# Kernel tuning notes

Hardware: AMD Instinct MI355X
Metric: run time of the kernel (lower is better)

The kernel has to match this reference:

```python
import jax, jax.numpy as jnp
import numpy as np

NUM_EMB = 100000
EMB = 64
NUM_CTNS = 10
HEADS = 4
ATT = 32
HD = HEADS * ATT  # 128
FIELDS = 32       # 20 onehot + 2 multihot + 10 ctns
B = 8192


def _linear_params(key, out_f, in_f):
    kw, kb = jax.random.split(key)
    W = jax.random.normal(kw, (out_f, in_f), jnp.float32) * 0.05
    b = jax.random.normal(kb, (out_f,), jnp.float32) * 0.05
    return W, b


def setup_inputs() -> dict:
    key = jax.random.key(0)
    ks = jax.random.split(key, 16)
    inp = {
        'onehot_i': jax.random.randint(ks[0], (B, 20), 0, NUM_EMB),
        'onehot_x': jax.random.uniform(ks[1], (B, 20), jnp.float32),
        'mh_i': jax.random.randint(ks[2], (2, B, 50), 0, NUM_EMB),
        'mh_x': jax.random.uniform(ks[3], (2, B, 50), jnp.float32),
        'ctns': jax.random.normal(ks[4], (B, NUM_CTNS), jnp.float32),
        'xx': jax.random.normal(ks[5], (NUM_EMB, EMB), jnp.float32),
        'xy': jax.random.normal(ks[6], (NUM_CTNS, EMB), jnp.float32),
    }
    # layer 1 attention params (emb -> h*d)
    names1 = ['QW1', 'Qb1', 'KW1', 'Kb1', 'VW1', 'Vb1', 'RW1', 'Rb1']
    for i in range(4):
        W, b = _linear_params(ks[7 + i], HD, EMB)
        inp[names1[2 * i]] = W
        inp[names1[2 * i + 1]] = b
    # layer 2 attention params (h*d -> h*d)
    names2 = ['QW2', 'Qb2', 'KW2', 'Kb2', 'VW2', 'Vb2', 'RW2', 'Rb2']
    for i in range(4):
        W, b = _linear_params(ks[11 + i], HD, HD)
        inp[names2[2 * i]] = W
        inp[names2[2 * i + 1]] = b
    lW, lb = _linear_params(ks[15], 1, FIELDS * HD)
    inp['logitW'] = lW
    inp['logitb'] = lb
    return inp


def _attn_block(y, QW, Qb, KW, Kb, VW, Vb, RW, Rb):
    # y: [B, F, D]; heads are head-major in the h*d output dim (matches torch split/cat)
    b, f, _ = y.shape
    Q = (y @ QW.T + Qb).reshape(b, f, HEADS, ATT)
    K = (y @ KW.T + Kb).reshape(b, f, HEADS, ATT)
    V = (y @ VW.T + Vb).reshape(b, f, HEADS, ATT)
    Res = y @ RW.T + Rb
    scores = jnp.einsum('bqhd,bkhd->bhqk', Q, K)  # unscaled, as in source
    A = jax.nn.softmax(scores, axis=-1)
    O = jnp.einsum('bhqk,bkhd->bqhd', A, V).reshape(b, f, HD)
    return jax.nn.relu(O + Res)


def reference(onehot_i, onehot_x, mh_i, mh_x, ctns, xx, xy,
              QW1, Qb1, KW1, Kb1, VW1, Vb1, RW1, Rb1,
              QW2, Qb2, KW2, Kb2, VW2, Vb2, RW2, Rb2,
              logitW, logitb):
    onehot_fields = xx[onehot_i] * onehot_x[..., None]                 # [B,20,EMB]
    mh_fields = (xx[mh_i] * mh_x[..., None]).sum(axis=2)               # [2,B,EMB]
    mh_fields = jnp.transpose(mh_fields, (1, 0, 2))                    # [B,2,EMB]
    ctns_fields = ctns[..., None] * xy                                 # [B,10,EMB]
    y = jnp.concatenate([onehot_fields, mh_fields, ctns_fields], axis=1)  # [B,32,EMB]
    y = _attn_block(y, QW1, Qb1, KW1, Kb1, VW1, Vb1, RW1, Rb1)
    y = _attn_block(y, QW2, Qb2, KW2, Kb2, VW2, Vb2, RW2, Rb2)
    flat = y.reshape(y.shape[0], -1)                                   # [B, 32*128]
    out = jax.nn.sigmoid(flat @ logitW.T + logitb)
    return out.squeeze()
```

## Files before the change

kernel.cpp:

```cpp
#include <hip/hip_runtime.h>
#include <hip/hip_bf16.h>


#define NSAMP 8192
#define S_Y1 72
#define S_Y2 136
#define S_T 36

typedef __attribute__((ext_vector_type(8))) short bf8_t;
typedef __attribute__((ext_vector_type(16))) float f16v;

__device__ __forceinline__ short f2bf(float f) {
  unsigned u = __float_as_uint(f);
  u += 0x7fffu + ((u >> 16) & 1u);
  return (short)(u >> 16);
}
__device__ __forceinline__ unsigned pack2(float a, float b) {
  __hip_bfloat162 h = __float22bfloat162_rn(float2{a, b});
  union { __hip_bfloat162 h2; unsigned u; } cvt;
  cvt.h2 = h;
  return cvt.u;
}
__device__ __forceinline__ float bf2f(short s) {
  return __uint_as_float(((unsigned)(unsigned short)s) << 16);
}
__device__ __forceinline__ float rcp_fast(float x) {
  return __builtin_amdgcn_rcpf(x);
}
__device__ __forceinline__ f16v mfma32(bf8_t a, bf8_t b, f16v c) {
  return __builtin_amdgcn_mfma_f32_32x32x16_bf16(a, b, c, 0, 0, 0);
}

template<int D>
__device__ __forceinline__ void proj2(const bf8_t (&af)[2][D / 16],
                                      const short* __restrict__ W,
                                      const float* __restrict__ bias,
                                      int fragBase, int n0, int col, f16v (&o)[2]) {
  float bb = bias[n0 + col];
#pragma unroll
  for (int i = 0; i < 16; ++i) { o[0][i] = bb; o[1][i] = bb; }
#pragma unroll
  for (int kc = 0; kc < D / 16; ++kc) {
    bf8_t w = *(const bf8_t*)&W[fragBase + kc * 512];
    o[0] = mfma32(af[0][kc], w, o[0]);
    o[1] = mfma32(af[1][kc], w, o[1]);
  }
}

__device__ __forceinline__ void storeQuad(short* tile, int stride, int g, int h2,
                                          int col, float a0, float a1, float a2,
                                          float a3) {
  unsigned p01 = pack2(a0, a1);
  unsigned p23 = pack2(a2, a3);
  int rb = 8 * g + 4 * h2;
  tile[(rb + 0) * stride + col] = (short)(p01 & 0xffffu);
  tile[(rb + 1) * stride + col] = (short)(p01 >> 16);
  tile[(rb + 2) * stride + col] = (short)(p23 & 0xffffu);
  tile[(rb + 3) * stride + col] = (short)(p23 >> 16);
}

template<int D_IN, int S_IN, bool FUSE>
__device__ void attn_layer(const short* yIn0, const short* yIn1,
                           short* yOut0, short* yOut1,
                           const short* __restrict__ Wq, const short* __restrict__ Wk,
                           const short* __restrict__ Wv, const short* __restrict__ Wr,
                           const float* __restrict__ bq, const float* __restrict__ bk,
                           const float* __restrict__ bvp, const float* __restrict__ br,
                           short* bQ0, short* bK0, short* bQ1, short* bK1,
                           const short* __restrict__ lwF,
                           int n0, int col, int h2, float (&pp)[2]) {
  constexpr int KS = D_IN / 16;
  const short* yIn[2] = {yIn0, yIn1};
  short* bQ[2] = {bQ0, bQ1};
  short* bK[2] = {bK0, bK1};
  const int head = n0 >> 5;
  const int lane = h2 * 32 + col;
  const int fragBase = head * KS * 512 + lane * 8;

  bf8_t af[2][KS];
#pragma unroll
  for (int sp = 0; sp < 2; ++sp)
#pragma unroll
    for (int kc = 0; kc < KS; ++kc)
      af[sp][kc] = *(const bf8_t*)&yIn[sp][col * S_IN + kc * 16 + h2 * 8];
  __syncthreads();

  f16v acc[2];

  proj2<D_IN>(af, Wq, bq, fragBase, n0, col, acc);
#pragma unroll
  for (int sp = 0; sp < 2; ++sp)
#pragma unroll
    for (int g = 0; g < 4; ++g)
      storeQuad(bQ[sp], S_T, g, h2, col, acc[sp][4 * g + 0], acc[sp][4 * g + 1],
                acc[sp][4 * g + 2], acc[sp][4 * g + 3]);

  proj2<D_IN>(af, Wk, bk, fragBase, n0, col, acc);
#pragma unroll
  for (int sp = 0; sp < 2; ++sp)
#pragma unroll
    for (int g = 0; g < 4; ++g)
      storeQuad(bK[sp], S_T, g, h2, col, acc[sp][4 * g + 0], acc[sp][4 * g + 1],
                acc[sp][4 * g + 2], acc[sp][4 * g + 3]);

  f16v res[2];
  proj2<D_IN>(af, Wr, br, fragBase, n0, col, res);

#pragma unroll
  for (int sp = 0; sp < 2; ++sp) {
    f16v z;
#pragma unroll
    for (int i = 0; i < 16; ++i) z[i] = 0.f;
#pragma unroll
    for (int kc = 0; kc < 2; ++kc) {
      bf8_t qa = *(const bf8_t*)&bQ[sp][col * S_T + kc * 16 + h2 * 8];
      bf8_t kb = *(const bf8_t*)&bK[sp][col * S_T + kc * 16 + h2 * 8];
      z = mfma32(qa, kb, z);
    }
#pragma unroll
    for (int g = 0; g < 4; ++g)
      storeQuad(bQ[sp], S_T, g, h2, col,
                __expf(z[4 * g + 0]), __expf(z[4 * g + 1]),
                __expf(z[4 * g + 2]), __expf(z[4 * g + 3]));
  }

  proj2<D_IN>(af, Wv, bvp, fragBase, n0, col, acc);
#pragma unroll
  for (int sp = 0; sp < 2; ++sp)
#pragma unroll
    for (int g = 0; g < 4; ++g) {
      uint2 pk;
      pk.x = pack2(acc[sp][g * 4 + 0], acc[sp][g * 4 + 1]);
      pk.y = pack2(acc[sp][g * 4 + 2], acc[sp][g * 4 + 3]);
      *(uint2*)&bK[sp][col * S_T + 8 * g + 4 * h2] = pk;
    }

  const short onebf = (short)0x3F80;
  bf8_t ones = {onebf, onebf, onebf, onebf, onebf, onebf, onebf, onebf};
  f16v pv[2], sums[2];
#pragma unroll
  for (int sp = 0; sp < 2; ++sp) {
#pragma unroll
    for (int i = 0; i < 16; ++i) { pv[sp][i] = 0.f; sums[sp][i] = 0.f; }
#pragma unroll
    for (int kc = 0; kc < 2; ++kc) {
      bf8_t pa = *(const bf8_t*)&bQ[sp][col * S_T + kc * 16 + h2 * 8];
      bf8_t vb = *(const bf8_t*)&bK[sp][col * S_T + kc * 16 + h2 * 8];
      pv[sp] = mfma32(pa, vb, pv[sp]);
      sums[sp] = mfma32(pa, ones, sums[sp]);
    }
  }

  if (FUSE) {
#pragma unroll
    for (int g = 0; g < 4; ++g) {
      short4 l4 = *(const short4*)&lwF[(head * 4 + g) * 256 + lane * 4];
#pragma unroll
      for (int r = 0; r < 4; ++r) {
        int reg = g * 4 + r;
        float lw = bf2f((r == 0) ? l4.x : (r == 1) ? l4.y : (r == 2) ? l4.z : l4.w);
        pp[0] += fmaxf(fmaf(pv[0][reg], rcp_fast(sums[0][reg]), res[0][reg]), 0.f) * lw;
        pp[1] += fmaxf(fmaf(pv[1][reg], rcp_fast(sums[1][reg]), res[1][reg]), 0.f) * lw;
      }
    }
  } else {
    __syncthreads();
    short* yOut[2] = {yOut0, yOut1};
#pragma unroll
    for (int sp = 0; sp < 2; ++sp)
#pragma unroll
      for (int g = 0; g < 4; ++g) {
        float v0 = fmaxf(fmaf(pv[sp][4 * g + 0], rcp_fast(sums[sp][4 * g + 0]),
                              res[sp][4 * g + 0]), 0.f);
        float v1 = fmaxf(fmaf(pv[sp][4 * g + 1], rcp_fast(sums[sp][4 * g + 1]),
                              res[sp][4 * g + 1]), 0.f);
        float v2 = fmaxf(fmaf(pv[sp][4 * g + 2], rcp_fast(sums[sp][4 * g + 2]),
                              res[sp][4 * g + 2]), 0.f);
        float v3 = fmaxf(fmaf(pv[sp][4 * g + 3], rcp_fast(sums[sp][4 * g + 3]),
                              res[sp][4 * g + 3]), 0.f);
        storeQuad(yOut[sp], S_Y2, g, h2, n0 + col, v0, v1, v2, v3);
      }
  }
}

__global__ __launch_bounds__(256, 3) void autoint_main(
    const int* __restrict__ onehot_i, const float* __restrict__ onehot_x,
    const int* __restrict__ mh_i, const float* __restrict__ mh_x,
    const float* __restrict__ ctns, const float* __restrict__ xx,
    const float* __restrict__ xy,
    const float* __restrict__ bq1, const float* __restrict__ bk1,
    const float* __restrict__ bv1, const float* __restrict__ br1,
    const float* __restrict__ bq2, const float* __restrict__ bk2,
    const float* __restrict__ bv2, const float* __restrict__ br2,
    const float* __restrict__ logitb, const short* __restrict__ wbf,
    float* __restrict__ out) {
  __shared__ __align__(16) short scr[2][9216];
  __shared__ float red[4][2];

  const int t = threadIdx.x;
  const int head = t >> 6;
  const int lane = t & 63;
  const int col = lane & 31;
  const int h2 = lane >> 5;
  const int n0 = head * 32;
  const int s0 = blockIdx.x * 2;

  short* bQ0 = &scr[0][(head * 2 + 0) * 1152];
  short* bK0 = &scr[0][(head * 2 + 1) * 1152];
  short* bQ1 = &scr[1][(head * 2 + 0) * 1152];
  short* bK1 = &scr[1][(head * 2 + 1) * 1152];

  int*   mhi_s = (int*)  &scr[0][2304];
  float* mhx_s = (float*)&scr[0][2704];

  int oh_r[2][2]; float oh_w[2][2];
  {
    const int f0 = t >> 4;
#pragma unroll
    for (int se = 0; se < 2; ++se) {
      oh_r[0][se] = onehot_i[(s0 + se) * 20 + f0];
      oh_w[0][se] = onehot_x[(s0 + se) * 20 + f0];
    }
    if (t < 64) {
      const int f1 = 16 + (t >> 4);
#pragma unroll
      for (int se = 0; se < 2; ++se) {
        oh_r[1][se] = onehot_i[(s0 + se) * 20 + f1];
        oh_w[1][se] = onehot_x[(s0 + se) * 20 + f1];
      }
    }
    if (t < 200) {
      int g = t / 50, k = t - g * 50;
      int se = g >> 1, j = g & 1;
      mhi_s[(se * 2 + j) * 50 + k] = mh_i[(j * NSAMP + s0 + se) * 50 + k];
      mhx_s[(se * 2 + j) * 50 + k] = mh_x[(j * NSAMP + s0 + se) * 50 + k];
    }
  }
  __syncthreads();

  {
    const int slot = t >> 3, ks = t & 7;
    const int j = slot >> 4, e4m = slot & 15;
#pragma unroll
    for (int se = 0; se < 2; ++se) {
      const int base = (se * 2 + j) * 50;
      float4 xv[7]; float wt[7];
#pragma unroll
      for (int i = 0; i < 7; ++i) {
        int k = ks + 8 * i;
        int ok = (k < 50);
        int row = ok ? mhi_s[base + k] : 0;
        wt[i] = ok ? mhx_s[base + k] : 0.f;
        xv[i] = *(const float4*)&xx[row * 64 + e4m * 4];
      }
      float a0 = 0.f, a1 = 0.f, a2 = 0.f, a3 = 0.f;
#pragma unroll
      for (int i = 0; i < 7; ++i) {
        a0 += xv[i].x * wt[i]; a1 += xv[i].y * wt[i];
        a2 += xv[i].z * wt[i]; a3 += xv[i].w * wt[i];
      }
#pragma unroll
      for (int d = 1; d < 8; d <<= 1) {
        a0 += __shfl_xor(a0, d); a1 += __shfl_xor(a1, d);
        a2 += __shfl_xor(a2, d); a3 += __shfl_xor(a3, d);
      }
      if (ks == 0) {
        uint2 w; w.x = pack2(a0, a1); w.y = pack2(a2, a3);
        *(uint2*)&scr[se][(20 + j) * S_Y1 + e4m * 4] = w;
      }
    }
  }

  {
    const int e4 = t & 15, f0 = t >> 4;
#pragma unroll
    for (int se = 0; se < 2; ++se) {
      float4 xv = *(const float4*)&xx[oh_r[0][se] * 64 + e4 * 4];
      float xw = oh_w[0][se];
      uint2 w; w.x = pack2(xv.x * xw, xv.y * xw); w.y = pack2(xv.z * xw, xv.w * xw);
      *(uint2*)&scr[se][f0 * S_Y1 + e4 * 4] = w;
    }
    if (t < 64) {
      const int f1 = 16 + (t >> 4);
#pragma unroll
      for (int se = 0; se < 2; ++se) {
        float4 xv = *(const float4*)&xx[oh_r[1][se] * 64 + e4 * 4];
        float xw = oh_w[1][se];
        uint2 w; w.x = pack2(xv.x * xw, xv.y * xw); w.y = pack2(xv.z * xw, xv.w * xw);
        *(uint2*)&scr[se][f1 * S_Y1 + e4 * 4] = w;
      }
    }
  }

  if (t < 160) {
    int ci = t >> 4, e4c = t & 15;
    float4 xv = *(const float4*)&xy[ci * 64 + e4c * 4];
    float cv0 = ctns[(s0 + 0) * 10 + ci];
    float cv1 = ctns[(s0 + 1) * 10 + ci];
    uint2 w0; w0.x = pack2(cv0 * xv.x, cv0 * xv.y); w0.y = pack2(cv0 * xv.z, cv0 * xv.w);
    *(uint2*)&scr[0][(22 + ci) * S_Y1 + e4c * 4] = w0;
    uint2 w1; w1.x = pack2(cv1 * xv.x, cv1 * xv.y); w1.y = pack2(cv1 * xv.z, cv1 * xv.w);
    *(uint2*)&scr[1][(22 + ci) * S_Y1 + e4c * 4] = w1;
  }
  __syncthreads();

  float pp[2] = {0.f, 0.f};
  attn_layer<64, S_Y1, false>(&scr[0][0], &scr[1][0], &scr[0][0], &scr[1][0],
      wbf + 0, wbf + 8192, wbf + 16384, wbf + 24576,
      bq1, bk1, bv1, br1, bQ0, bK0, bQ1, bK1, nullptr, n0, col, h2, pp);
  __syncthreads();
  attn_layer<128, S_Y2, true>(&scr[0][0], &scr[1][0], nullptr, nullptr,
      wbf + 32768, wbf + 49152, wbf + 65536, wbf + 81920,
      bq2, bk2, bv2, br2, bQ0, bK0, bQ1, bK1, wbf + 98304, n0, col, h2, pp);

#pragma unroll
  for (int off = 32; off > 0; off >>= 1) {
    pp[0] += __shfl_xor(pp[0], off);
    pp[1] += __shfl_xor(pp[1], off);
  }
  if (lane == 0) { red[head][0] = pp[0]; red[head][1] = pp[1]; }
  __syncthreads();
  if (t < 2) {
    float zz = red[0][t] + red[1][t] + red[2][t] + red[3][t] + logitb[0];
    out[s0 + t] = 1.f / (1.f + __expf(-zz));
  }
}

__global__ void convert_w(const float* __restrict__ qw1, const float* __restrict__ kw1,
                          const float* __restrict__ vw1, const float* __restrict__ rw1,
                          const float* __restrict__ qw2, const float* __restrict__ kw2,
                          const float* __restrict__ vw2, const float* __restrict__ rw2,
                          const float* __restrict__ lw, short* __restrict__ outw) {
  int i = blockIdx.x * 256 + threadIdx.x;
  if (i >= 102400) return;
  float v;
  if (i < 32768) {
    int tsel = i >> 13, d = i & 8191;
    int e = d & 7, lane = (d >> 3) & 63, kc = (d >> 9) & 3, h = (d >> 11) & 3;
    int col = lane & 31, h2 = lane >> 5;
    int j = (h * 32 + col) * 64 + kc * 16 + h2 * 8 + e;
    const float* src = tsel == 0 ? qw1 : tsel == 1 ? kw1 : tsel == 2 ? vw1 : rw1;
    v = src[j];
  } else if (i < 98304) {
    int k = i - 32768;
    int tsel = k >> 14, d = k & 16383;
    int e = d & 7, lane = (d >> 3) & 63, kc = (d >> 9) & 7, h = (d >> 12) & 3;
    int col = lane & 31, h2 = lane >> 5;
    int j = (h * 32 + col) * 128 + kc * 16 + h2 * 8 + e;
    const float* src = tsel == 0 ? qw2 : tsel == 1 ? kw2 : tsel == 2 ? vw2 : rw2;
    v = src[j];
  } else {
    int d = i - 98304;
    int r = d & 3, lane = (d >> 2) & 63, g = (d >> 8) & 3, h = (d >> 10) & 3;
    int col = lane & 31, h2 = lane >> 5;
    v = lw[(8 * g + 4 * h2 + r) * 128 + h * 32 + col];
  }
  outw[i] = f2bf(v);
}

extern "C" void kernel_launch(void* const* d_in, const int* in_sizes, int n_in,
                              void* d_out, int out_size, void* d_ws, size_t ws_size,
                              hipStream_t stream) {
  short* wbf = (short*)d_ws;
  convert_w<<<400, 256, 0, stream>>>(
      (const float*)d_in[7], (const float*)d_in[9], (const float*)d_in[11],
      (const float*)d_in[13], (const float*)d_in[15], (const float*)d_in[17],
      (const float*)d_in[19], (const float*)d_in[21], (const float*)d_in[23], wbf);
  autoint_main<<<NSAMP / 2, 256, 0, stream>>>(
      (const int*)d_in[0], (const float*)d_in[1], (const int*)d_in[2],
      (const float*)d_in[3], (const float*)d_in[4], (const float*)d_in[5],
      (const float*)d_in[6],
      (const float*)d_in[8], (const float*)d_in[10], (const float*)d_in[12],
      (const float*)d_in[14], (const float*)d_in[16], (const float*)d_in[18],
      (const float*)d_in[20], (const float*)d_in[22], (const float*)d_in[24],
      wbf, (float*)d_out);
}
```

Before: 259.2 us.

## Software-prefetch next projection weights and reorder embedding gathers for latency overlap

Each projection now loads the first four weight fragments of the next projection (including the first layer-2 Q weights during the layer-1 V projection) into registers while it runs its MFMAs. The first layer-1 weights are loaded at kernel start. The onehot embedding gathers are issued before the multihot reduction so their latency overlaps it, the continuous-feature writes move before the first barrier, and the logit weights are loaded before the PV MFMAs. The aim is to hide global-memory latency in a kernel that stalls on serialized loads, at the cost of extra VGPRs that could lower occupancy.

```diff
diff --git a/kernel.cpp b/kernel.cpp
--- a/kernel.cpp
+++ b/kernel.cpp
@@ -31,19 +31,35 @@
   return __builtin_amdgcn_mfma_f32_32x32x16_bf16(a, b, c, 0, 0, 0);
 }
 
-template<int D>
-__device__ __forceinline__ void proj2(const bf8_t (&af)[2][D / 16],
-                                      const short* __restrict__ W,
-                                      const float* __restrict__ bias,
-                                      int fragBase, int n0, int col, f16v (&o)[2]) {
+template<int KS, bool HAS_NEXT>
+__device__ __forceinline__ void projPF(const bf8_t (&af)[2][KS],
+                                       const short* __restrict__ W,
+                                       const float* __restrict__ bias,
+                                       int fragBase,
+                                       const short* __restrict__ Wnext,
+                                       int fbNext, int n0, int col,
+                                       bf8_t (&pre)[4], f16v (&o)[2]) {
+  constexpr int PF = (KS < 4) ? KS : 4;
+  bf8_t nxt[4];
+  if constexpr (HAS_NEXT) {
+#pragma unroll
+    for (int i = 0; i < 4; ++i)
+      nxt[i] = *(const bf8_t*)&Wnext[fbNext + i * 512];
+  }
   float bb = bias[n0 + col];
 #pragma unroll
   for (int i = 0; i < 16; ++i) { o[0][i] = bb; o[1][i] = bb; }
 #pragma unroll
-  for (int kc = 0; kc < D / 16; ++kc) {
-    bf8_t w = *(const bf8_t*)&W[fragBase + kc * 512];
+  for (int kc = 0; kc < KS; ++kc) {
+    bf8_t w;
+    if (kc < PF) w = pre[kc];
+    else w = *(const bf8_t*)&W[fragBase + kc * 512];
     o[0] = mfma32(af[0][kc], w, o[0]);
     o[1] = mfma32(af[1][kc], w, o[1]);
+  }
+  if constexpr (HAS_NEXT) {
+#pragma unroll
+    for (int i = 0; i < 4; ++i) pre[i] = nxt[i];
   }
 }
 
@@ -68,7 +84,9 @@
                            const float* __restrict__ bvp, const float* __restrict__ br,
                            short* bQ0, short* bK0, short* bQ1, short* bK1,
                            const short* __restrict__ lwF,
-                           int n0, int col, int h2, float (&pp)[2]) {
+                           const short* __restrict__ WnlQ, int fbNext,
+                           int n0, int col, int h2, bf8_t (&pre)[4],
+                           float (&pp)[2]) {
   constexpr int KS = D_IN / 16;
   const short* yIn[2] = {yIn0, yIn1};
   short* bQ[2] = {bQ0, bQ1};
@@ -87,7 +105,7 @@
 
   f16v acc[2];
 
-  proj2<D_IN>(af, Wq, bq, fragBase, n0, col, acc);
+  projPF<KS, true>(af, Wq, bq, fragBase, Wk, fragBase, n0, col, pre, acc);
 #pragma unroll
   for (int sp = 0; sp < 2; ++sp)
 #pragma unroll
@@ -95,7 +113,7 @@
       storeQuad(bQ[sp], S_T, g, h2, col, acc[sp][4 * g + 0], acc[sp][4 * g + 1],
                 acc[sp][4 * g + 2], acc[sp][4 * g + 3]);
 
-  proj2<D_IN>(af, Wk, bk, fragBase, n0, col, acc);
+  projPF<KS, true>(af, Wk, bk, fragBase, Wr, fragBase, n0, col, pre, acc);
 #pragma unroll
   for (int sp = 0; sp < 2; ++sp)
 #pragma unroll
@@ -104,7 +122,7 @@
                 acc[sp][4 * g + 2], acc[sp][4 * g + 3]);
 
   f16v res[2];
-  proj2<D_IN>(af, Wr, br, fragBase, n0, col, res);
+  projPF<KS, true>(af, Wr, br, fragBase, Wv, fragBase, n0, col, pre, res);
 
 #pragma unroll
   for (int sp = 0; sp < 2; ++sp) {
@@ -124,7 +142,7 @@
                 __expf(z[4 * g + 2]), __expf(z[4 * g + 3]));
   }
 
-  proj2<D_IN>(af, Wv, bvp, fragBase, n0, col, acc);
+  projPF<KS, !FUSE>(af, Wv, bvp, fragBase, WnlQ, fbNext, n0, col, pre, acc);
 #pragma unroll
   for (int sp = 0; sp < 2; ++sp)
 #pragma unroll
@@ -135,6 +153,13 @@
       *(uint2*)&bK[sp][col * S_T + 8 * g + 4 * h2] = pk;
     }
 
+  short4 l4b[4];
+  if constexpr (FUSE) {
+#pragma unroll
+    for (int g = 0; g < 4; ++g)
+      l4b[g] = *(const short4*)&lwF[(head * 4 + g) * 256 + lane * 4];
+  }
+
   const short onebf = (short)0x3F80;
   bf8_t ones = {onebf, onebf, onebf, onebf, onebf, onebf, onebf, onebf};
   f16v pv[2], sums[2];
@@ -151,10 +176,10 @@
     }
   }
 
-  if (FUSE) {
+  if constexpr (FUSE) {
 #pragma unroll
     for (int g = 0; g < 4; ++g) {
-      short4 l4 = *(const short4*)&lwF[(head * 4 + g) * 256 + lane * 4];
+      short4 l4 = l4b[g];
 #pragma unroll
       for (int r = 0; r < 4; ++r) {
         int reg = g * 4 + r;
@@ -210,33 +235,57 @@
   short* bQ1 = &scr[1][(head * 2 + 0) * 1152];
   short* bK1 = &scr[1][(head * 2 + 1) * 1152];
 
+  const int fb1 = head * 4 * 512 + lane * 8;
+  const int fb2 = head * 8 * 512 + lane * 8;
+  bf8_t pre[4];
+#pragma unroll
+  for (int i = 0; i < 4; ++i) pre[i] = *(const bf8_t*)&wbf[fb1 + i * 512];
+
   int*   mhi_s = (int*)  &scr[0][2304];
   float* mhx_s = (float*)&scr[0][2704];
 
+  const int e4 = t & 15, f0 = t >> 4;
+
   int oh_r[2][2]; float oh_w[2][2];
-  {
-    const int f0 = t >> 4;
+#pragma unroll
+  for (int se = 0; se < 2; ++se) {
+    oh_r[0][se] = onehot_i[(s0 + se) * 20 + f0];
+    oh_w[0][se] = onehot_x[(s0 + se) * 20 + f0];
+  }
+  if (t < 64) {
 #pragma unroll
     for (int se = 0; se < 2; ++se) {
-      oh_r[0][se] = onehot_i[(s0 + se) * 20 + f0];
-      oh_w[0][se] = onehot_x[(s0 + se) * 20 + f0];
-    }
-    if (t < 64) {
-      const int f1 = 16 + (t >> 4);
-#pragma unroll
-      for (int se = 0; se < 2; ++se) {
-        oh_r[1][se] = onehot_i[(s0 + se) * 20 + f1];
-        oh_w[1][se] = onehot_x[(s0 + se) * 20 + f1];
-      }
-    }
-    if (t < 200) {
-      int g = t / 50, k = t - g * 50;
-      int se = g >> 1, j = g & 1;
-      mhi_s[(se * 2 + j) * 50 + k] = mh_i[(j * NSAMP + s0 + se) * 50 + k];
-      mhx_s[(se * 2 + j) * 50 + k] = mh_x[(j * NSAMP + s0 + se) * 50 + k];
-    }
+      oh_r[1][se] = onehot_i[(s0 + se) * 20 + 16 + f0];
+      oh_w[1][se] = onehot_x[(s0 + se) * 20 + 16 + f0];
+    }
+  }
+  if (t < 160) {
+    int ci = t >> 4;
+    float4 xv = *(const float4*)&xy[ci * 64 + e4 * 4];
+    float cv0 = ctns[(s0 + 0) * 10 + ci];
+    float cv1 = ctns[(s0 + 1) * 10 + ci];
+    uint2 w0; w0.x = pack2(cv0 * xv.x, cv0 * xv.y); w0.y = pack2(cv0 * xv.z, cv0 * xv.w);
+    *(uint2*)&scr[0][(22 + ci) * S_Y1 + e4 * 4] = w0;
+    uint2 w1; w1.x = pack2(cv1 * xv.x, cv1 * xv.y); w1.y = pack2(cv1 * xv.z, cv1 * xv.w);
+    *(uint2*)&scr[1][(22 + ci) * S_Y1 + e4 * 4] = w1;
+  }
+  if (t < 200) {
+    int g = t / 50, k = t - g * 50;
+    int se = g >> 1, j = g & 1;
+    mhi_s[(se * 2 + j) * 50 + k] = mh_i[(j * NSAMP + s0 + se) * 50 + k];
+    mhx_s[(se * 2 + j) * 50 + k] = mh_x[(j * NSAMP + s0 + se) * 50 + k];
   }
   __syncthreads();
+
+  float4 g0[2], g1[2];
+#pragma unroll
+  for (int se = 0; se < 2; ++se)
+    g0[se] = *(const float4*)&xx[oh_r[0][se] * 64 + e4 * 4];
+  if (t < 64) {
+#pragma unroll
+    for (int se = 0; se < 2; ++se)
+      g1[se] = *(const float4*)&xx[oh_r[1][se] * 64 + e4 * 4];
+  }
 
   {
     const int slot = t >> 3, ks = t & 7;
@@ -271,47 +320,34 @@
     }
   }
 
-  {
-    const int e4 = t & 15, f0 = t >> 4;
+#pragma unroll
+  for (int se = 0; se < 2; ++se) {
+    float xw = oh_w[0][se];
+    uint2 w; w.x = pack2(g0[se].x * xw, g0[se].y * xw);
+    w.y = pack2(g0[se].z * xw, g0[se].w * xw);
+    *(uint2*)&scr[se][f0 * S_Y1 + e4 * 4] = w;
+  }
+  if (t < 64) {
 #pragma unroll
     for (int se = 0; se < 2; ++se) {
-      float4 xv = *(const float4*)&xx[oh_r[0][se] * 64 + e4 * 4];
-      float xw = oh_w[0][se];
-      uint2 w; w.x = pack2(xv.x * xw, xv.y * xw); w.y = pack2(xv.z * xw, xv.w * xw);
-      *(uint2*)&scr[se][f0 * S_Y1 + e4 * 4] = w;
-    }
-    if (t < 64) {
-      const int f1 = 16 + (t >> 4);
-#pragma unroll
-      for (int se = 0; se < 2; ++se) {
-        float4 xv = *(const float4*)&xx[oh_r[1][se] * 64 + e4 * 4];
-        float xw = oh_w[1][se];
-        uint2 w; w.x = pack2(xv.x * xw, xv.y * xw); w.y = pack2(xv.z * xw, xv.w * xw);
-        *(uint2*)&scr[se][f1 * S_Y1 + e4 * 4] = w;
-      }
-    }
-  }
-
-  if (t < 160) {
-    int ci = t >> 4, e4c = t & 15;
-    float4 xv = *(const float4*)&xy[ci * 64 + e4c * 4];
-    float cv0 = ctns[(s0 + 0) * 10 + ci];
-    float cv1 = ctns[(s0 + 1) * 10 + ci];
-    uint2 w0; w0.x = pack2(cv0 * xv.x, cv0 * xv.y); w0.y = pack2(cv0 * xv.z, cv0 * xv.w);
-    *(uint2*)&scr[0][(22 + ci) * S_Y1 + e4c * 4] = w0;
-    uint2 w1; w1.x = pack2(cv1 * xv.x, cv1 * xv.y); w1.y = pack2(cv1 * xv.z, cv1 * xv.w);
-    *(uint2*)&scr[1][(22 + ci) * S_Y1 + e4c * 4] = w1;
+      float xw = oh_w[1][se];
+      uint2 w; w.x = pack2(g1[se].x * xw, g1[se].y * xw);
+      w.y = pack2(g1[se].z * xw, g1[se].w * xw);
+      *(uint2*)&scr[se][(16 + f0) * S_Y1 + e4 * 4] = w;
+    }
   }
   __syncthreads();
 
   float pp[2] = {0.f, 0.f};
   attn_layer<64, S_Y1, false>(&scr[0][0], &scr[1][0], &scr[0][0], &scr[1][0],
       wbf + 0, wbf + 8192, wbf + 16384, wbf + 24576,
-      bq1, bk1, bv1, br1, bQ0, bK0, bQ1, bK1, nullptr, n0, col, h2, pp);
+      bq1, bk1, bv1, br1, bQ0, bK0, bQ1, bK1, nullptr,
+      wbf + 32768, fb2, n0, col, h2, pre, pp);
   __syncthreads();
   attn_layer<128, S_Y2, true>(&scr[0][0], &scr[1][0], nullptr, nullptr,
       wbf + 32768, wbf + 49152, wbf + 65536, wbf + 81920,
-      bq2, bk2, bv2, br2, bQ0, bK0, bQ1, bK1, wbf + 98304, n0, col, h2, pp);
+      bq2, bk2, bv2, br2, bQ0, bK0, bQ1, bK1, wbf + 98304,
+      wbf, 0, n0, col, h2, pre, pp);
 
 #pragma unroll
   for (int off = 32; off > 0; off >>= 1) {
```

After: 256.6 us. Within noise of the previous version (-1.0%).
